# Kernel optimization log

Measured on AMD Instinct MI355X. Metric: run time of the kernel, lower is better.

The kernel has to match this reference:

```python
import jax, jax.numpy as jnp
import numpy as np

COMMITMENT_COST = 0.25
N, D, K = 131072, 64, 1024


def setup_inputs() -> dict:
    key = jax.random.key(0)
    k1, k2 = jax.random.split(key)
    inputs = jax.random.normal(k1, (N, D), dtype=jnp.float32)
    # torch init: uniform(-1/K, 1/K)
    weight = jax.random.uniform(k2, (K, D), dtype=jnp.float32,
                                minval=-1.0 / K, maxval=1.0 / K)
    return {"inputs": inputs, "weight": weight}


def reference(inputs, weight):
    x2 = jnp.sum(inputs * inputs, axis=1, keepdims=True)          # [N, 1]
    e2 = jnp.sum(weight * weight, axis=1)                          # [K]
    distances = x2 + e2 - 2.0 * jnp.matmul(inputs, weight.T)       # [N, K]
    encoding_indices = jnp.argmin(distances, axis=1)               # [N]
    # scatter one-hot + matmul in the original == direct gather
    quantized = jnp.take(weight, encoding_indices, axis=0)         # [N, D]
    e_latent_loss = jnp.mean((jax.lax.stop_gradient(quantized) - inputs) ** 2)
    q_latent_loss = jnp.mean((quantized - jax.lax.stop_gradient(inputs)) ** 2)
    loss = q_latent_loss + COMMITMENT_COST * e_latent_loss
    # straight-through estimator
    quantized_st = inputs + jax.lax.stop_gradient(quantized - inputs)
    return (quantized_st, loss, encoding_indices)
```

## Files before the change

### kernel.cpp

```cpp
#include <hip/hip_runtime.h>


#define NROWS 131072
#define DIM 64
#define KCODES 1024
#define MARGIN 5e-5f
#define LOSS_SCALE (1.25f / ((float)NROWS * (float)DIM))
#define BSTRIDE 72

typedef short bf16x8 __attribute__((ext_vector_type(8)));
typedef float f32x4 __attribute__((ext_vector_type(4)));

__device__ __forceinline__ short f2bf(float f) {
    unsigned u = __float_as_uint(f);
    u += 0x7FFF + ((u >> 16) & 1);
    return (short)(u >> 16);
}
__device__ __forceinline__ float bf2f(short h) {
    return __uint_as_float(((unsigned)(unsigned short)h) << 16);
}

__global__ __launch_bounds__(256) void prep_w(const float* __restrict__ w,
                                              float* __restrict__ e2,
                                              short* __restrict__ w_hi,
                                              short* __restrict__ w_lo) {
    int k = blockIdx.x * blockDim.x + threadIdx.x;
    if (k >= KCODES) return;
    const float* wk = w + (size_t)k * DIM;
    float s = 0.f;
#pragma unroll
    for (int d = 0; d < DIM; ++d) {
        float f = wk[d];
        s = fmaf(f, f, s);
        short hi = f2bf(f);
        w_hi[(size_t)k * DIM + d] = hi;
        w_lo[(size_t)k * DIM + d] = f2bf(f - bf2f(hi));
    }
    e2[k] = s;
}

__global__ __launch_bounds__(256, 2) void vq_main(
        const float* __restrict__ x, const float* __restrict__ w,
        const float* __restrict__ e2,
        const short* __restrict__ w_hi, const short* __restrict__ w_lo,
        float* __restrict__ out_q, float* __restrict__ out_loss,
        float* __restrict__ out_idx,
        unsigned* __restrict__ flag_cnt, unsigned* __restrict__ flag_list) {
    const int tid = threadIdx.x;
    const int lane = tid & 63;
    const int wv = tid >> 6;
    const int m = lane & 15;
    const int q = lane >> 4;
    const int block_row0 = blockIdx.x * 128;
    const int wave_row0 = block_row0 + wv * 32;

    __shared__ short sb[2][32 * BSTRIDE];
    __shared__ int sidx[128];
    __shared__ unsigned char sflg[128];
    __shared__ float red[4];

    float xa[2][2][8];
#pragma unroll
    for (int rt = 0; rt < 2; ++rt) {
        const float* xr = x + (size_t)(wave_row0 + rt * 16 + m) * DIM + q * 8;
        *(float4*)&xa[rt][0][0] = *(const float4*)(xr);
        *(float4*)&xa[rt][0][4] = *(const float4*)(xr + 4);
        *(float4*)&xa[rt][1][0] = *(const float4*)(xr + 32);
        *(float4*)&xa[rt][1][4] = *(const float4*)(xr + 36);
    }
    float x2m[2];
#pragma unroll
    for (int rt = 0; rt < 2; ++rt) {
        float s = 0.f;
#pragma unroll
        for (int c = 0; c < 2; ++c)
#pragma unroll
            for (int j = 0; j < 8; ++j) s = fmaf(xa[rt][c][j], xa[rt][c][j], s);
        s += __shfl_xor(s, 16, 64);
        s += __shfl_xor(s, 32, 64);
        x2m[rt] = s;
    }
    float x2e[2][4];
#pragma unroll
    for (int rt = 0; rt < 2; ++rt)
#pragma unroll
        for (int r = 0; r < 4; ++r)
            x2e[rt][r] = __shfl(x2m[rt], (lane & 48) + q * 4 + r, 64);

    bf16x8 ah[2][2], al[2][2];
#pragma unroll
    for (int rt = 0; rt < 2; ++rt)
#pragma unroll
        for (int c = 0; c < 2; ++c)
#pragma unroll
            for (int j = 0; j < 8; ++j) {
                float f = xa[rt][c][j];
                short h = f2bf(f);
                ah[rt][c][j] = h;
                al[rt][c][j] = f2bf(f - bf2f(h));
            }

    float best[2][4], sec[2][4];
    int bidx[2][4];
#pragma unroll
    for (int rt = 0; rt < 2; ++rt)
#pragma unroll
        for (int r = 0; r < 4; ++r) {
            best[rt][r] = 3.4e38f;
            sec[rt][r] = 3.4e38f;
            bidx[rt][r] = 0;
        }

    for (int t = 0; t < KCODES / 32; ++t) {
        __syncthreads();
#pragma unroll
        for (int i = 0; i < 2; ++i) {
            int ch = tid + i * 256;
            int arr = ch >> 8;
            int code = (ch >> 3) & 31;
            int seg = ch & 7;
            const short* src = (arr ? w_lo : w_hi) +
                               ((size_t)(t * 32 + code)) * DIM + seg * 8;
            *(bf16x8*)&sb[arr][code * BSTRIDE + seg * 8] = *(const bf16x8*)src;
        }
        __syncthreads();

        bf16x8 bh[2][2], bl[2][2];
#pragma unroll
        for (int ct = 0; ct < 2; ++ct)
#pragma unroll
            for (int kc = 0; kc < 2; ++kc) {
                int off = (ct * 16 + m) * BSTRIDE + kc * 32 + q * 8;
                bh[ct][kc] = *(bf16x8*)&sb[0][off];
                bl[ct][kc] = *(bf16x8*)&sb[1][off];
            }

        f32x4 acc[2][2];
#pragma unroll
        for (int rt = 0; rt < 2; ++rt)
#pragma unroll
            for (int ct = 0; ct < 2; ++ct) {
                f32x4 a = {0.f, 0.f, 0.f, 0.f};
                a = __builtin_amdgcn_mfma_f32_16x16x32_bf16(al[rt][0], bh[ct][0], a, 0, 0, 0);
                a = __builtin_amdgcn_mfma_f32_16x16x32_bf16(ah[rt][0], bl[ct][0], a, 0, 0, 0);
                a = __builtin_amdgcn_mfma_f32_16x16x32_bf16(ah[rt][0], bh[ct][0], a, 0, 0, 0);
                a = __builtin_amdgcn_mfma_f32_16x16x32_bf16(al[rt][1], bh[ct][1], a, 0, 0, 0);
                a = __builtin_amdgcn_mfma_f32_16x16x32_bf16(ah[rt][1], bl[ct][1], a, 0, 0, 0);
                a = __builtin_amdgcn_mfma_f32_16x16x32_bf16(ah[rt][1], bh[ct][1], a, 0, 0, 0);
                acc[rt][ct] = a;
            }

        float e2c0 = e2[t * 32 + m];
        float e2c1 = e2[t * 32 + 16 + m];
#pragma unroll
        for (int rt = 0; rt < 2; ++rt)
#pragma unroll
            for (int ct = 0; ct < 2; ++ct) {
                float e2c = ct ? e2c1 : e2c0;
                int id = t * 32 + ct * 16 + m;
#pragma unroll
                for (int r = 0; r < 4; ++r) {
                    float d = fmaf(-2.f, acc[rt][ct][r], x2e[rt][r] + e2c);
                    bool c = d < best[rt][r];
                    sec[rt][r] = fminf(sec[rt][r], fmaxf(d, best[rt][r]));
                    if (c) { best[rt][r] = d; bidx[rt][r] = id; }
                }
            }
    }

#pragma unroll
    for (int off = 1; off < 16; off <<= 1)
#pragma unroll
        for (int rt = 0; rt < 2; ++rt)
#pragma unroll
            for (int r = 0; r < 4; ++r) {
                float ob = __shfl_xor(best[rt][r], off, 64);
                int oi = __shfl_xor(bidx[rt][r], off, 64);
                float os = __shfl_xor(sec[rt][r], off, 64);
                float mx = fmaxf(best[rt][r], ob);
                sec[rt][r] = fminf(fminf(sec[rt][r], os), mx);
                bool take = (ob < best[rt][r]) ||
                            (ob == best[rt][r] && oi < bidx[rt][r]);
                if (take) { best[rt][r] = ob; bidx[rt][r] = oi; }
            }

    if (m == 0) {
#pragma unroll
        for (int rt = 0; rt < 2; ++rt)
#pragma unroll
            for (int r = 0; r < 4; ++r) {
                int lr = wv * 32 + rt * 16 + q * 4 + r;
                sidx[lr] = bidx[rt][r];
                bool fl = (sec[rt][r] - best[rt][r]) < MARGIN;
                sflg[lr] = fl ? 1 : 0;
                if (fl) {
                    unsigned p = atomicAdd(flag_cnt, 1u);
                    flag_list[p] = (unsigned)(block_row0 + lr);
                }
            }
    }
    __syncthreads();

    float lsum = 0.f;
    const int rl = tid >> 2, part = tid & 3;
#pragma unroll
    for (int p = 0; p < 2; ++p) {
        int lr = p * 64 + rl;
        int grow = block_row0 + lr;
        if (!sflg[lr]) {
            int bi = sidx[lr];
            const float* xs = x + (size_t)grow * DIM + part * 16;
            const float* ws = w + (size_t)bi * DIM + part * 16;
            float* os = out_q + (size_t)grow * DIM + part * 16;
#pragma unroll
            for (int i = 0; i < 4; ++i) {
                float4 xv = *(const float4*)(xs + 4 * i);
                float4 wv4 = *(const float4*)(ws + 4 * i);
                float d0 = wv4.x - xv.x, d1 = wv4.y - xv.y;
                float d2 = wv4.z - xv.z, d3 = wv4.w - xv.w;
                lsum = fmaf(d0, d0, lsum);
                lsum = fmaf(d1, d1, lsum);
                lsum = fmaf(d2, d2, lsum);
                lsum = fmaf(d3, d3, lsum);
                float4 o = {xv.x + d0, xv.y + d1, xv.z + d2, xv.w + d3};
                *(float4*)(os + 4 * i) = o;
            }
            if (part == 0) out_idx[grow] = (float)bi;
        }
    }

    for (int off = 32; off > 0; off >>= 1) lsum += __shfl_down(lsum, off, 64);
    if ((tid & 63) == 0) red[tid >> 6] = lsum;
    __syncthreads();
    if (tid == 0) {
        float s = (red[0] + red[1]) + (red[2] + red[3]);
        atomicAdd(out_loss, s * LOSS_SCALE);
    }
}

#define CH 16
__global__ __launch_bounds__(256) void vq_cleanup(
        const float* __restrict__ x, const float* __restrict__ w,
        const float* __restrict__ e2,
        const unsigned* __restrict__ flag_cnt,
        const unsigned* __restrict__ flag_list,
        float* __restrict__ out_q, float* __restrict__ out_loss,
        float* __restrict__ out_idx) {
    __shared__ float xs[CH][68];
    __shared__ float wt[128][68];
    __shared__ float sx2[CH];
    const int tid = threadIdx.x;
    const int rowsub = tid >> 4;
    const int kslot = tid & 15;
    const unsigned cnt = *flag_cnt;

    for (unsigned base = blockIdx.x * CH; base < cnt; base += gridDim.x * CH) {
        const int nrows = (int)min((unsigned)CH, cnt - base);
        __syncthreads();
        {
            int rr = tid >> 4, sg = tid & 15;
            if (rr < nrows) {
                unsigned grow = flag_list[base + rr];
                *(float4*)&xs[rr][sg * 4] =
                    *(const float4*)(x + (size_t)grow * DIM + sg * 4);
            }
        }
        __syncthreads();
        if (tid < nrows) {
            float s = 0.f;
#pragma unroll
            for (int d = 0; d < DIM; ++d) s = fmaf(xs[tid][d], xs[tid][d], s);
            sx2[tid] = s;
        }

        unsigned long long kmin = ~0ULL;
        for (int tile = 0; tile < KCODES / 128; ++tile) {
            __syncthreads();
#pragma unroll
            for (int i = 0; i < 8; ++i) {
                int f = tid + i * 256;
                int code = f >> 4, sg = f & 15;
                *(float4*)&wt[code][sg * 4] =
                    *(const float4*)(w + (size_t)(tile * 128 + code) * DIM + sg * 4);
            }
            __syncthreads();
            if (rowsub < nrows) {
#pragma unroll
                for (int j = 0; j < 8; ++j) {
                    int cl = j * 16 + kslot;
                    int code = tile * 128 + cl;
                    float dot = 0.f;
#pragma unroll
                    for (int d = 0; d < DIM; ++d)
                        dot = fmaf(wt[cl][d], xs[rowsub][d], dot);
                    float dist = (sx2[rowsub] + e2[code]) - 2.0f * dot;
                    unsigned long long key =
                        ((unsigned long long)__float_as_uint(dist) << 32) |
                        (unsigned)code;
                    kmin = kmin < key ? kmin : key;
                }
            }
        }
#pragma unroll
        for (int off = 1; off < 16; off <<= 1) {
            unsigned long long o = __shfl_xor(kmin, off, 64);
            kmin = kmin < o ? kmin : o;
        }
        if (rowsub < nrows) {
            unsigned long long kk = __shfl(kmin, (tid & 63) & ~15, 64);
            int bi = (int)(unsigned)(kk & 0xFFFFFFFFu);
            unsigned grow = flag_list[base + rowsub];
            float4 x4 = *(float4*)&xs[rowsub][kslot * 4];
            float4 w4 = *(const float4*)(w + (size_t)bi * DIM + kslot * 4);
            float d0 = w4.x - x4.x, d1 = w4.y - x4.y;
            float d2 = w4.z - x4.z, d3 = w4.w - x4.w;
            float ls = 0.f;
            ls = fmaf(d0, d0, ls);
            ls = fmaf(d1, d1, ls);
            ls = fmaf(d2, d2, ls);
            ls = fmaf(d3, d3, ls);
            float4 o = {x4.x + d0, x4.y + d1, x4.z + d2, x4.w + d3};
            *(float4*)(out_q + (size_t)grow * DIM + kslot * 4) = o;
            if (kslot == 0) out_idx[grow] = (float)bi;
#pragma unroll
            for (int off = 1; off < 16; off <<= 1)
                ls += __shfl_xor(ls, off, 64);
            if (kslot == 0) atomicAdd(out_loss, ls * LOSS_SCALE);
        }
    }
}

extern "C" void kernel_launch(void* const* d_in, const int* in_sizes, int n_in,
                              void* d_out, int out_size, void* d_ws, size_t ws_size,
                              hipStream_t stream) {
    const float* x = (const float*)d_in[0];
    const float* w = (const float*)d_in[1];

    float* out_q    = (float*)d_out;
    float* out_loss = (float*)d_out + (size_t)NROWS * DIM;
    float* out_idx  = out_loss + 1;

    float* e2 = (float*)d_ws;
    short* w_hi = (short*)(e2 + KCODES);
    short* w_lo = w_hi + (size_t)KCODES * DIM;
    unsigned* cnt = (unsigned*)(w_lo + (size_t)KCODES * DIM);
    unsigned* list = cnt + 1;

    hipMemsetAsync(out_loss, 0, sizeof(float), stream);
    hipMemsetAsync(cnt, 0, sizeof(unsigned), stream);

    prep_w<<<(KCODES + 255) / 256, 256, 0, stream>>>(w, e2, w_hi, w_lo);
    vq_main<<<NROWS / 128, 256, 0, stream>>>(x, w, e2, w_hi, w_lo,
                                             out_q, out_loss, out_idx, cnt, list);
    vq_cleanup<<<512, 256, 0, stream>>>(x, w, e2, cnt, list,
                                        out_q, out_loss, out_idx);
}
```

Measured before the change: 222.8 us.

## Pre-swizzle codebook into MFMA fragment layout and load directly from global

prep_w now writes the bf16 hi/lo codebook in the exact per-lane MFMA fragment order, so vq_main loads B operands straight from global/L2 instead of staging them through shared memory with two barriers per tile. The per-row |x|^2 term is dropped from the argmin distance because it is constant per row, and occupancy is raised to 3 blocks per CU. The cleanup kernel gets vectorised LDS dot products, drops a redundant shuffle, and runs on half as many blocks. The risk is more global/L2 traffic per wave, and the margin-based second-best flagging now compares distances without x2, which keeps the gaps unchanged but alters the magnitude scale.

```diff
diff --git a/kernel.cpp b/kernel.cpp
--- a/kernel.cpp
+++ b/kernel.cpp
@@ -6,7 +6,6 @@
 #define KCODES 1024
 #define MARGIN 5e-5f
 #define LOSS_SCALE (1.25f / ((float)NROWS * (float)DIM))
-#define BSTRIDE 72
 
 typedef short bf16x8 __attribute__((ext_vector_type(8)));
 typedef float f32x4 __attribute__((ext_vector_type(4)));
@@ -27,19 +26,34 @@
     int k = blockIdx.x * blockDim.x + threadIdx.x;
     if (k >= KCODES) return;
     const float* wk = w + (size_t)k * DIM;
+    float r[DIM];
+#pragma unroll
+    for (int i = 0; i < DIM / 4; ++i) *(float4*)&r[4 * i] = *(const float4*)(wk + 4 * i);
     float s = 0.f;
 #pragma unroll
-    for (int d = 0; d < DIM; ++d) {
-        float f = wk[d];
-        s = fmaf(f, f, s);
-        short hi = f2bf(f);
-        w_hi[(size_t)k * DIM + d] = hi;
-        w_lo[(size_t)k * DIM + d] = f2bf(f - bf2f(hi));
-    }
+    for (int d = 0; d < DIM; ++d) s = fmaf(r[d], r[d], s);
     e2[k] = s;
-}
-
-__global__ __launch_bounds__(256, 2) void vq_main(
+
+    const int t = k >> 5, ct = (k >> 4) & 1, m = k & 15;
+#pragma unroll
+    for (int kc = 0; kc < 2; ++kc)
+#pragma unroll
+        for (int q = 0; q < 4; ++q) {
+            bf16x8 hv, lv;
+#pragma unroll
+            for (int j = 0; j < 8; ++j) {
+                float f = r[kc * 32 + q * 8 + j];
+                short h = f2bf(f);
+                hv[j] = h;
+                lv[j] = f2bf(f - bf2f(h));
+            }
+            size_t fo = ((size_t)(((t * 2 + ct) * 2 + kc) * 4 + q) * 16 + m) * 8;
+            *(bf16x8*)(w_hi + fo) = hv;
+            *(bf16x8*)(w_lo + fo) = lv;
+        }
+}
+
+__global__ __launch_bounds__(256, 3) void vq_main(
         const float* __restrict__ x, const float* __restrict__ w,
         const float* __restrict__ e2,
         const short* __restrict__ w_hi, const short* __restrict__ w_lo,
@@ -54,7 +68,6 @@
     const int block_row0 = blockIdx.x * 128;
     const int wave_row0 = block_row0 + wv * 32;
 
-    __shared__ short sb[2][32 * BSTRIDE];
     __shared__ int sidx[128];
     __shared__ unsigned char sflg[128];
     __shared__ float red[4];
@@ -68,25 +81,6 @@
         *(float4*)&xa[rt][1][0] = *(const float4*)(xr + 32);
         *(float4*)&xa[rt][1][4] = *(const float4*)(xr + 36);
     }
-    float x2m[2];
-#pragma unroll
-    for (int rt = 0; rt < 2; ++rt) {
-        float s = 0.f;
-#pragma unroll
-        for (int c = 0; c < 2; ++c)
-#pragma unroll
-            for (int j = 0; j < 8; ++j) s = fmaf(xa[rt][c][j], xa[rt][c][j], s);
-        s += __shfl_xor(s, 16, 64);
-        s += __shfl_xor(s, 32, 64);
-        x2m[rt] = s;
-    }
-    float x2e[2][4];
-#pragma unroll
-    for (int rt = 0; rt < 2; ++rt)
-#pragma unroll
-        for (int r = 0; r < 4; ++r)
-            x2e[rt][r] = __shfl(x2m[rt], (lane & 48) + q * 4 + r, 64);
-
     bf16x8 ah[2][2], al[2][2];
 #pragma unroll
     for (int rt = 0; rt < 2; ++rt)
@@ -111,29 +105,21 @@
             bidx[rt][r] = 0;
         }
 
+    const short* ph = w_hi + q * 128 + m * 8;
+    const short* pl = w_lo + q * 128 + m * 8;
+
     for (int t = 0; t < KCODES / 32; ++t) {
-        __syncthreads();
-#pragma unroll
-        for (int i = 0; i < 2; ++i) {
-            int ch = tid + i * 256;
-            int arr = ch >> 8;
-            int code = (ch >> 3) & 31;
-            int seg = ch & 7;
-            const short* src = (arr ? w_lo : w_hi) +
-                               ((size_t)(t * 32 + code)) * DIM + seg * 8;
-            *(bf16x8*)&sb[arr][code * BSTRIDE + seg * 8] = *(const bf16x8*)src;
-        }
-        __syncthreads();
-
         bf16x8 bh[2][2], bl[2][2];
 #pragma unroll
         for (int ct = 0; ct < 2; ++ct)
 #pragma unroll
             for (int kc = 0; kc < 2; ++kc) {
-                int off = (ct * 16 + m) * BSTRIDE + kc * 32 + q * 8;
-                bh[ct][kc] = *(bf16x8*)&sb[0][off];
-                bl[ct][kc] = *(bf16x8*)&sb[1][off];
-            }
+                int off = t * 2048 + (ct * 2 + kc) * 512;
+                bh[ct][kc] = *(const bf16x8*)(ph + off);
+                bl[ct][kc] = *(const bf16x8*)(pl + off);
+            }
+        float e2c0 = e2[t * 32 + m];
+        float e2c1 = e2[t * 32 + 16 + m];
 
         f32x4 acc[2][2];
 #pragma unroll
@@ -150,8 +136,6 @@
                 acc[rt][ct] = a;
             }
 
-        float e2c0 = e2[t * 32 + m];
-        float e2c1 = e2[t * 32 + 16 + m];
 #pragma unroll
         for (int rt = 0; rt < 2; ++rt)
 #pragma unroll
@@ -160,10 +144,10 @@
                 int id = t * 32 + ct * 16 + m;
 #pragma unroll
                 for (int r = 0; r < 4; ++r) {
-                    float d = fmaf(-2.f, acc[rt][ct][r], x2e[rt][r] + e2c);
-                    bool c = d < best[rt][r];
-                    sec[rt][r] = fminf(sec[rt][r], fmaxf(d, best[rt][r]));
-                    if (c) { best[rt][r] = d; bidx[rt][r] = id; }
+                    float g = fmaf(-2.f, acc[rt][ct][r], e2c);
+                    bool c = g < best[rt][r];
+                    sec[rt][r] = fminf(sec[rt][r], fmaxf(g, best[rt][r]));
+                    if (c) { best[rt][r] = g; bidx[rt][r] = id; }
                 }
             }
     }
@@ -291,8 +275,14 @@
                     int code = tile * 128 + cl;
                     float dot = 0.f;
 #pragma unroll
-                    for (int d = 0; d < DIM; ++d)
-                        dot = fmaf(wt[cl][d], xs[rowsub][d], dot);
+                    for (int d4 = 0; d4 < 16; ++d4) {
+                        float4 wv4 = *(const float4*)&wt[cl][d4 * 4];
+                        float4 xv4 = *(const float4*)&xs[rowsub][d4 * 4];
+                        dot = fmaf(wv4.x, xv4.x, dot);
+                        dot = fmaf(wv4.y, xv4.y, dot);
+                        dot = fmaf(wv4.z, xv4.z, dot);
+                        dot = fmaf(wv4.w, xv4.w, dot);
+                    }
                     float dist = (sx2[rowsub] + e2[code]) - 2.0f * dot;
                     unsigned long long key =
                         ((unsigned long long)__float_as_uint(dist) << 32) |
@@ -307,8 +297,7 @@
             kmin = kmin < o ? kmin : o;
         }
         if (rowsub < nrows) {
-            unsigned long long kk = __shfl(kmin, (tid & 63) & ~15, 64);
-            int bi = (int)(unsigned)(kk & 0xFFFFFFFFu);
+            int bi = (int)(unsigned)(kmin & 0xFFFFFFFFu);
             unsigned grow = flag_list[base + rowsub];
             float4 x4 = *(float4*)&xs[rowsub][kslot * 4];
             float4 w4 = *(const float4*)(w + (size_t)bi * DIM + kslot * 4);
@@ -352,6 +341,6 @@
     prep_w<<<(KCODES + 255) / 256, 256, 0, stream>>>(w, e2, w_hi, w_lo);
     vq_main<<<NROWS / 128, 256, 0, stream>>>(x, w, e2, w_hi, w_lo,
                                              out_q, out_loss, out_idx, cnt, list);
-    vq_cleanup<<<512, 256, 0, stream>>>(x, w, e2, cnt, list,
+    vq_cleanup<<<256, 256, 0, stream>>>(x, w, e2, cnt, list,
                                         out_q, out_loss, out_idx);
 }
```

After: 208.7 us. 6.3% less time.
